# Kernel optimization log

Measured on AMD Instinct MI355X. Metric: run time of the kernel, lower is better.

The kernel has to match this reference:

```python
import jax, jax.numpy as jnp
import numpy as np

S, B, C, H = 1024, 4, 1024, 16
CC = C // H


def setup_inputs() -> dict:
    key = jax.random.key(0)
    ks = jax.random.split(key, 10)
    scale = 1.0 / np.sqrt(C)
    return {
        "x": jax.random.normal(ks[0], (S, B, C), dtype=jnp.float32),
        "r": jax.random.normal(ks[1], (S, B, C), dtype=jnp.float32),
        "Wq": jax.random.normal(ks[2], (C, C), dtype=jnp.float32) * scale,
        "bq": jnp.zeros((C,), dtype=jnp.float32),
        "Wke": jax.random.normal(ks[3], (C, C), dtype=jnp.float32) * scale,
        "bke": jnp.zeros((C,), dtype=jnp.float32),
        "Wkr": jax.random.normal(ks[4], (C, C), dtype=jnp.float32) * scale,
        "bkr": jnp.zeros((C,), dtype=jnp.float32),
        "u": jax.random.normal(ks[5], (C,), dtype=jnp.float32) * 0.02,
        "v": jax.random.normal(ks[6], (C,), dtype=jnp.float32) * 0.02,
    }


def reference(x, r, Wq, bq, Wke, bke, Wkr, bkr, u, v):
    s, b, c = x.shape
    h, cc = H, CC
    # projections (torch Linear: y = x @ W^T + b)
    ewq = (x @ Wq.T + bq).reshape(s, b, h, cc)
    ewke_full = x @ Wke.T + bke                 # [s,b,c]
    ewke = ewke_full.reshape(s, b, h, cc)
    rwkr_full = r @ Wkr.T + bkr                 # [s,b,c]
    rwkr = rwkr_full.reshape(s, b, h, cc)
    # content-content and content-position terms
    term_a = jnp.einsum('sbnc,tbnc->stbn', ewq, ewke)
    term_b = jnp.einsum('sbnc,tbnc->stbn', ewq, rwkr)
    # global bias terms: uwke/vwke are constant over (s,b), so the stb einsum
    # reduces to a tb contraction broadcast over s (same math, no s*b copies)
    uwke = Wke @ u + bke                        # [c]
    vwke = Wkr @ v + bkr                        # [c]
    term_c = jnp.einsum('c,tbc->tb', uwke, ewke_full)   # [t,b]
    term_d = jnp.einsum('c,tbc->tb', vwke, rwkr_full)   # [t,b]
    bias = (term_c + term_d)[None, :, :, None]          # [1,t,b,1]
    return term_a + term_b + bias               # [s,t,b,h]
```

## Files before the change

### kernel.cpp

```cpp
#include <hip/hip_runtime.h>
#include <hip/hip_bf16.h>
#include <stdint.h>

#define Ssz 1024
#define Bsz 4
#define Csz 1024
#define Hsz 16
#define Msz 4096

typedef unsigned short u16;
typedef __attribute__((ext_vector_type(8))) short bf16x8;
typedef __attribute__((ext_vector_type(8))) unsigned short u16x8;
typedef __attribute__((ext_vector_type(4))) float f32x4;
typedef __attribute__((ext_vector_type(4))) unsigned short u16x4;

__device__ __forceinline__ u16 f2bf(float f) {
  union { float f; unsigned u; } x; x.f = f;
  unsigned r = x.u + 0x7fffu + ((x.u >> 16) & 1u);
  return (u16)(r >> 16);
}

__device__ __forceinline__ void glds16(const void* g, void* l) {
  __builtin_amdgcn_global_load_lds(
      (__attribute__((address_space(1))) void*)g,
      (__attribute__((address_space(3))) void*)l, 16, 0, 0);
}

__device__ __forceinline__ int swzb(int x) { return x ^ (((x >> 8) & 7) << 4); }

__global__ __launch_bounds__(256) void k_convert_w(
    const float* __restrict__ Wq, const float* __restrict__ Wke, const float* __restrict__ Wkr,
    const float* __restrict__ bke, const float* __restrict__ bkr,
    const float* __restrict__ uu, const float* __restrict__ vv,
    u16* __restrict__ Bq, u16* __restrict__ B2, float* __restrict__ biasK,
    float* __restrict__ uwke, float* __restrict__ vwke) {
  int c = blockIdx.x;
  int tid = threadIdx.x;
  int c4 = tid * 4;
  float4 q = *(const float4*)(Wq + (size_t)c * Csz + c4);
  float4 e = *(const float4*)(Wke + (size_t)c * Csz + c4);
  float4 k = *(const float4*)(Wkr + (size_t)c * Csz + c4);
  u16x4 qo = { f2bf(q.x), f2bf(q.y), f2bf(q.z), f2bf(q.w) };
  u16x4 eo = { f2bf(e.x), f2bf(e.y), f2bf(e.z), f2bf(e.w) };
  u16x4 ko = { f2bf(k.x), f2bf(k.y), f2bf(k.z), f2bf(k.w) };
  *(u16x4*)(Bq + (size_t)c * 1024 + c4) = qo;
  *(u16x4*)(B2 + (size_t)c * 2048 + c4) = eo;
  *(u16x4*)(B2 + (size_t)c * 2048 + 1024 + c4) = ko;
  float4 u4 = *(const float4*)(uu + c4);
  float4 v4 = *(const float4*)(vv + c4);
  float se = e.x * u4.x + e.y * u4.y + e.z * u4.z + e.w * u4.w;
  float sk = k.x * v4.x + k.y * v4.y + k.z * v4.z + k.w * v4.w;
  for (int m = 32; m; m >>= 1) { se += __shfl_xor(se, m); sk += __shfl_xor(sk, m); }
  __shared__ float red[2][4];
  if ((tid & 63) == 0) { red[0][tid >> 6] = se; red[1][tid >> 6] = sk; }
  __syncthreads();
  if (tid == 0) {
    uwke[c] = red[0][0] + red[0][1] + red[0][2] + red[0][3] + bke[c];
    vwke[c] = red[1][0] + red[1][1] + red[1][2] + red[1][3] + bkr[c];
    biasK[c] = bke[c] + bkr[c];
  }
}

__global__ __launch_bounds__(256) void k_prep2(
    const float* __restrict__ Wke, const float* __restrict__ Wkr,
    const float* __restrict__ uwke, const float* __restrict__ vwke,
    const float* __restrict__ bke, const float* __restrict__ bkr,
    float* __restrict__ wu, float* __restrict__ wv, float* __restrict__ cst) {
  int bid = blockIdx.x;
  int tid = threadIdx.x;
  if (bid < 64) {
    const float* W = (bid < 32) ? Wke : Wkr;
    const float* sv = (bid < 32) ? uwke : vwke;
    float* o = (bid < 32) ? wu : wv;
    int d = (bid & 31) * 32 + (tid & 31);
    int cpar = tid >> 5;
    float acc = 0.f;
    #pragma unroll 8
    for (int c = cpar; c < Csz; c += 8) acc += sv[c] * W[(size_t)c * Csz + d];
    __shared__ float red[8][32];
    red[cpar][tid & 31] = acc;
    __syncthreads();
    if (cpar == 0) {
      float s = 0.f;
      #pragma unroll
      for (int i = 0; i < 8; i++) s += red[i][tid & 31];
      o[d] = s;
    }
  } else {
    float s = 0.f;
    for (int i = tid; i < Csz; i += 256) s += uwke[i] * bke[i] + vwke[i] * bkr[i];
    for (int m = 32; m; m >>= 1) s += __shfl_xor(s, m);
    __shared__ float red1[4];
    if ((tid & 63) == 0) red1[tid >> 6] = s;
    __syncthreads();
    if (tid == 0) cst[0] = red1[0] + red1[1] + red1[2] + red1[3];
  }
}

__global__ __launch_bounds__(256) void k_convert_xr_bias(
    const float* __restrict__ x, const float* __restrict__ r,
    const float* __restrict__ wu, const float* __restrict__ wv,
    const float* __restrict__ cst, u16* __restrict__ A2, float* __restrict__ biasTB) {
  int m = blockIdx.x;
  int tid = threadIdx.x;
  int c4 = tid * 4;
  float4 xv = *(const float4*)(x + (size_t)m * Csz + c4);
  float4 rv = *(const float4*)(r + (size_t)m * Csz + c4);
  u16x4 xo = { f2bf(xv.x), f2bf(xv.y), f2bf(xv.z), f2bf(xv.w) };
  u16x4 ro = { f2bf(rv.x), f2bf(rv.y), f2bf(rv.z), f2bf(rv.w) };
  *(u16x4*)(A2 + (size_t)m * 2048 + c4) = xo;
  *(u16x4*)(A2 + (size_t)m * 2048 + 1024 + c4) = ro;
  float4 a = *(const float4*)(wu + c4);
  float4 b = *(const float4*)(wv + c4);
  float s = xv.x * a.x + xv.y * a.y + xv.z * a.z + xv.w * a.w
          + rv.x * b.x + rv.y * b.y + rv.z * b.z + rv.w * b.w;
  for (int mm = 32; mm; mm >>= 1) s += __shfl_xor(s, mm);
  __shared__ float red[4];
  if ((tid & 63) == 0) red[tid >> 6] = s;
  __syncthreads();
  if (tid == 0) biasTB[m] = red[0] + red[1] + red[2] + red[3] + cst[0];
}

__global__ __launch_bounds__(256, 3) void k_gemm(
    const u16* __restrict__ A2, const u16* __restrict__ Bq, const u16* __restrict__ B2,
    const float* __restrict__ bq, const float* __restrict__ biasK,
    u16* __restrict__ QF, u16* __restrict__ KF) {
  __shared__ u16 smem[24576];

  const int z = blockIdx.z;
  const u16* A = A2; const int lda = 2048;
  const u16* B = (z == 0) ? Bq : B2;
  const int ldb = (z == 0) ? 1024 : 2048;
  const float* bias = (z == 0) ? bq : biasK;
  u16* OF = (z == 0) ? QF : KF;
  const int NT = ((z == 0) ? 1024 : 2048) >> 5;

  const int tid = threadIdx.x;
  const int bm = blockIdx.y * 128, bn = blockIdx.x * 128;
  const int wave = tid >> 6, lane = tid & 63;
  const int wm = (wave & 1) * 64, wn = (wave >> 1) * 64;
  const int fr = lane & 15, kg = (lane >> 4) * 8;

  const int ch0 = tid, ch1 = 256 + tid;
  const int r0 = ch0 >> 2, c0 = (ch0 & 3) * 8;
  const int r1 = ch1 >> 2, c1 = (ch1 & 3) * 8;
  const u16* a0 = A + (size_t)(bm + r0) * lda + c0;
  const u16* a1 = A + (size_t)(bm + r1) * lda + c1;
  const u16* b0 = B + (size_t)(bn + r0) * ldb + c0;
  const u16* b1 = B + (size_t)(bn + r1) * ldb + c1;

  f32x4 acc[4][4] = {};

  glds16(a0, smem + ch0 * 8);           glds16(a1, smem + ch1 * 8);
  glds16(b0, smem + 4096 + ch0 * 8);    glds16(b1, smem + 4096 + ch1 * 8);
  glds16(a0 + 32, smem + 8192 + ch0 * 8);        glds16(a1 + 32, smem + 8192 + ch1 * 8);
  glds16(b0 + 32, smem + 8192 + 4096 + ch0 * 8); glds16(b1 + 32, smem + 8192 + 4096 + ch1 * 8);

  int cur = 0;
  for (int t = 0; t < NT; t++) {
    if (t == NT - 1) {
      asm volatile("s_waitcnt vmcnt(0)" ::: "memory");
    } else {
      asm volatile("s_waitcnt vmcnt(4)" ::: "memory");
    }
    __builtin_amdgcn_s_barrier();
    asm volatile("" ::: "memory");
    if (t + 2 < NT) {
      const int nxt = cur >= 1 ? cur - 1 : 2;
      u16* an = smem + nxt * 8192;
      u16* bn_ = an + 4096;
      const int kt = (t + 2) * 32;
      glds16(a0 + kt, an + ch0 * 8);   glds16(a1 + kt, an + ch1 * 8);
      glds16(b0 + kt, bn_ + ch0 * 8);  glds16(b1 + kt, bn_ + ch1 * 8);
    }
    const u16* ac = smem + cur * 8192;
    const u16* bc = ac + 4096;
    bf16x8 af[4], bf[4];
    #pragma unroll
    for (int mi = 0; mi < 4; mi++) af[mi] = *(const bf16x8*)(ac + (wm + mi * 16 + fr) * 32 + kg);
    #pragma unroll
    for (int ni = 0; ni < 4; ni++) bf[ni] = *(const bf16x8*)(bc + (wn + ni * 16 + fr) * 32 + kg);
    #pragma unroll
    for (int mi = 0; mi < 4; mi++)
      #pragma unroll
      for (int ni = 0; ni < 4; ni++)
        acc[mi][ni] = __builtin_amdgcn_mfma_f32_16x16x32_bf16(af[mi], bf[ni], acc[mi][ni], 0, 0, 0);
    cur = cur < 2 ? cur + 1 : 0;
  }
  __syncthreads();

  const int hi = lane >> 4;
  const int e8 = fr & 7;
  const int fr3 = fr >> 3;
  u16* epw = smem + wave * 4096;
  float bvn[4];
  #pragma unroll
  for (int ni = 0; ni < 4; ni++) bvn[ni] = bias[bn + wn + ni * 16 + fr];
  #pragma unroll
  for (int ni = 0; ni < 4; ni++) {
    const int kk = ni >> 1;
    const int g = (ni * 2 + fr3) & 3;
    #pragma unroll
    for (int mi = 0; mi < 4; mi++) {
      const int inner = (g * 16 + mi * 4 + hi) * 8 + e8;
      #pragma unroll
      for (int j = 0; j < 4; j++)
        epw[(j * 2 + kk) * 512 + inner] = f2bf(acc[mi][ni][j] + bvn[ni]);
    }
  }
  const int s_tile = (bm >> 6) + (wm >> 6);
  const int nh = (bn + wn) >> 6;
  #pragma unroll
  for (int p = 0; p < 8; p++) {
    const int b2 = p >> 1, kk = p & 1;
    u16x8 v = *(const u16x8*)(&epw[p * 512 + lane * 8]);
    size_t ci = ((size_t)(s_tile * 4 + b2) * 16 + nh) * 2 + kk;
    *(u16x8*)(OF + ci * 512 + lane * 8) = v;
  }
}

__global__ __launch_bounds__(256, 3) void k_attn(
    const u16* __restrict__ QF, const u16* __restrict__ KF,
    const float* __restrict__ biasTB, float* __restrict__ out) {
  int id = blockIdx.x;
  int xcd = id & 7, within = id >> 3;
  int sx = xcd & 3, tx = xcd >> 2;
  int panel = within >> 7;
  int pl = within & 127;
  int s_tile = sx * 16 + (pl >> 3);
  int t_tile = tx * 32 + panel * 8 + (pl & 7);
  int s0 = s_tile * 16, t0 = t_tile * 16;

  int tid = threadIdx.x;
  int wave = tid >> 6, lane = tid & 63;
  int fr = lane & 15;

  const u16* qp = QF + (size_t)(s_tile * 4 + wave) * 16384 + lane * 8;
  const u16* kp = KF + (size_t)(t_tile * 4 + wave) * 16384 + lane * 8;

  f32x4 acc[16];
  #pragma unroll
  for (int n = 0; n < 16; n++) acc[n] = (f32x4){0.f, 0.f, 0.f, 0.f};

  #pragma unroll
  for (int n = 0; n < 16; n++) {
    #pragma unroll
    for (int kk = 0; kk < 2; kk++) {
      bf16x8 a  = *(const bf16x8*)(qp + (n * 2 + kk) * 512);
      bf16x8 bb = *(const bf16x8*)(kp + (n * 2 + kk) * 512);
      acc[n] = __builtin_amdgcn_mfma_f32_16x16x32_bf16(a, bb, acc[n], 0, 0, 0);
    }
  }

  __shared__ float lds[8192];
  float bv = biasTB[(t0 + (tid >> 4)) * 4 + ((tid >> 2) & 3)];
  int hi = (lane >> 4) & 1;
  int myg = (lane >> 4) >> 1;

  #pragma unroll
  for (int g = 0; g < 2; g++) {
    __syncthreads();
    if (myg == g) {
      #pragma unroll
      for (int j = 0; j < 4; j++) {
        int lbase = (((hi * 4 + j) * 16 + fr) * 4 + wave) * 64;
        #pragma unroll
        for (int n0 = 0; n0 < 16; n0 += 4) {
          f32x4 v = { acc[n0][j], acc[n0 + 1][j], acc[n0 + 2][j], acc[n0 + 3][j] };
          *(f32x4*)((char*)lds + swzb(lbase + n0 * 4)) = v;
        }
      }
    }
    __syncthreads();
    #pragma unroll
    for (int sr = 0; sr < 8; sr++) {
      f32x4 v = *(const f32x4*)((char*)lds + swzb(sr * 4096 + tid * 16));
      v += bv;
      size_t off = ((size_t)(s0 + g * 8 + sr) * 1024 + t0) * 64 + tid * 4;
      __builtin_nontemporal_store(v, (f32x4*)(out + off));
    }
  }
}

extern "C" void kernel_launch(void* const* d_in, const int* in_sizes, int n_in,
                              void* d_out, int out_size, void* d_ws, size_t ws_size,
                              hipStream_t stream) {
  const float* x   = (const float*)d_in[0];
  const float* r   = (const float*)d_in[1];
  const float* Wq  = (const float*)d_in[2];
  const float* bq  = (const float*)d_in[3];
  const float* Wke = (const float*)d_in[4];
  const float* bke = (const float*)d_in[5];
  const float* Wkr = (const float*)d_in[6];
  const float* bkr = (const float*)d_in[7];
  const float* uu  = (const float*)d_in[8];
  const float* vv  = (const float*)d_in[9];
  float* out = (float*)d_out;
  char* ws = (char*)d_ws;

  u16* A2 = (u16*)(ws + 0);
  u16* QF = (u16*)(ws + 16777216);
  u16* KF = (u16*)(ws + 25165824);
  u16* B2 = (u16*)(ws + 33554432);
  u16* Bq = (u16*)(ws + 37748736);
  float* uwke  = (float*)(ws + 39845888);
  float* vwke  = (float*)(ws + 39849984);
  float* wu    = (float*)(ws + 39854080);
  float* wv    = (float*)(ws + 39858176);
  float* biasK = (float*)(ws + 39862272);
  float* cst   = (float*)(ws + 39866368);
  float* biasTB = (float*)(ws + 39866624);

  k_convert_w<<<1024, 256, 0, stream>>>(Wq, Wke, Wkr, bke, bkr, uu, vv,
                                        Bq, B2, biasK, uwke, vwke);
  k_prep2<<<65, 256, 0, stream>>>(Wke, Wkr, uwke, vwke, bke, bkr, wu, wv, cst);
  k_convert_xr_bias<<<4096, 256, 0, stream>>>(x, r, wu, wv, cst, A2, biasTB);
  k_gemm<<<dim3(8, 32, 2), 256, 0, stream>>>(A2, Bq, B2, bq, biasK, QF, KF);
  k_attn<<<4096, 256, 0, stream>>>(QF, KF, biasTB, out);
}
```

Before: 126.9 us.

## Compute two t-tiles per attention block to reuse Q fragments

Each k_attn block now computes a 16x32 (s,t) tile instead of 16x16, loading each Q fragment once and applying it to two K tiles, and the grid is halved to 2048 blocks. The epilogue is restructured into four LDS staging passes, each covering four s rows by 32 t columns, with separate bias values for the two t halves. This cuts redundant Q loads and per-block overhead, at the cost of double the accumulator registers (which can lower occupancy under launch_bounds 256,3) and more LDS sync rounds. The kernel is dominated by output stores, so the benefit is limited.

```diff
diff --git a/kernel.cpp b/kernel.cpp
--- a/kernel.cpp
+++ b/kernel.cpp
@@ -225,58 +225,70 @@
   int id = blockIdx.x;
   int xcd = id & 7, within = id >> 3;
   int sx = xcd & 3, tx = xcd >> 2;
-  int panel = within >> 7;
-  int pl = within & 127;
-  int s_tile = sx * 16 + (pl >> 3);
-  int t_tile = tx * 32 + panel * 8 + (pl & 7);
-  int s0 = s_tile * 16, t0 = t_tile * 16;
+  int panel = within >> 6;
+  int pl = within & 63;
+  int s_tile = sx * 16 + (pl >> 2);
+  int t2 = tx * 16 + panel * 4 + (pl & 3);
+  int s0 = s_tile * 16;
 
   int tid = threadIdx.x;
   int wave = tid >> 6, lane = tid & 63;
   int fr = lane & 15;
 
-  const u16* qp = QF + (size_t)(s_tile * 4 + wave) * 16384 + lane * 8;
-  const u16* kp = KF + (size_t)(t_tile * 4 + wave) * 16384 + lane * 8;
-
-  f32x4 acc[16];
-  #pragma unroll
-  for (int n = 0; n < 16; n++) acc[n] = (f32x4){0.f, 0.f, 0.f, 0.f};
-
+  const u16* qp  = QF + (size_t)(s_tile * 4 + wave) * 16384 + lane * 8;
+  const u16* kpA = KF + (size_t)((t2 * 2) * 4 + wave) * 16384 + lane * 8;
+  const u16* kpB = kpA + 4 * 16384;
+
+  f32x4 accA[16], accB[16];
   #pragma unroll
   for (int n = 0; n < 16; n++) {
-    #pragma unroll
-    for (int kk = 0; kk < 2; kk++) {
-      bf16x8 a  = *(const bf16x8*)(qp + (n * 2 + kk) * 512);
-      bf16x8 bb = *(const bf16x8*)(kp + (n * 2 + kk) * 512);
-      acc[n] = __builtin_amdgcn_mfma_f32_16x16x32_bf16(a, bb, acc[n], 0, 0, 0);
-    }
+    accA[n] = (f32x4){0.f, 0.f, 0.f, 0.f};
+    accB[n] = (f32x4){0.f, 0.f, 0.f, 0.f};
+  }
+
+  #pragma unroll
+  for (int n = 0; n < 16; n++) {
+    bf16x8 q0 = *(const bf16x8*)(qp + (n * 2 + 0) * 512);
+    bf16x8 q1 = *(const bf16x8*)(qp + (n * 2 + 1) * 512);
+    bf16x8 a0 = *(const bf16x8*)(kpA + (n * 2 + 0) * 512);
+    bf16x8 a1 = *(const bf16x8*)(kpA + (n * 2 + 1) * 512);
+    bf16x8 b0 = *(const bf16x8*)(kpB + (n * 2 + 0) * 512);
+    bf16x8 b1 = *(const bf16x8*)(kpB + (n * 2 + 1) * 512);
+    accA[n] = __builtin_amdgcn_mfma_f32_16x16x32_bf16(q0, a0, accA[n], 0, 0, 0);
+    accA[n] = __builtin_amdgcn_mfma_f32_16x16x32_bf16(q1, a1, accA[n], 0, 0, 0);
+    accB[n] = __builtin_amdgcn_mfma_f32_16x16x32_bf16(q0, b0, accB[n], 0, 0, 0);
+    accB[n] = __builtin_amdgcn_mfma_f32_16x16x32_bf16(q1, b1, accB[n], 0, 0, 0);
   }
 
   __shared__ float lds[8192];
-  float bv = biasTB[(t0 + (tid >> 4)) * 4 + ((tid >> 2) & 3)];
-  int hi = (lane >> 4) & 1;
-  int myg = (lane >> 4) >> 1;
-
-  #pragma unroll
-  for (int g = 0; g < 2; g++) {
+  float bv0 = biasTB[(t2 * 32 +      (tid >> 4)) * 4 + ((tid >> 2) & 3)];
+  float bv1 = biasTB[(t2 * 32 + 16 + (tid >> 4)) * 4 + ((tid >> 2) & 3)];
+  int hi = lane >> 4;
+
+  #pragma unroll
+  for (int p = 0; p < 4; p++) {
     __syncthreads();
-    if (myg == g) {
+    if (hi == p) {
       #pragma unroll
       for (int j = 0; j < 4; j++) {
-        int lbase = (((hi * 4 + j) * 16 + fr) * 4 + wave) * 64;
+        int lbaseA = ((j * 32 +      fr) * 4 + wave) * 64;
+        int lbaseB = ((j * 32 + 16 + fr) * 4 + wave) * 64;
         #pragma unroll
         for (int n0 = 0; n0 < 16; n0 += 4) {
-          f32x4 v = { acc[n0][j], acc[n0 + 1][j], acc[n0 + 2][j], acc[n0 + 3][j] };
-          *(f32x4*)((char*)lds + swzb(lbase + n0 * 4)) = v;
+          f32x4 vA = { accA[n0][j], accA[n0 + 1][j], accA[n0 + 2][j], accA[n0 + 3][j] };
+          f32x4 vB = { accB[n0][j], accB[n0 + 1][j], accB[n0 + 2][j], accB[n0 + 3][j] };
+          *(f32x4*)((char*)lds + swzb(lbaseA + n0 * 4)) = vA;
+          *(f32x4*)((char*)lds + swzb(lbaseB + n0 * 4)) = vB;
         }
       }
     }
     __syncthreads();
     #pragma unroll
-    for (int sr = 0; sr < 8; sr++) {
-      f32x4 v = *(const f32x4*)((char*)lds + swzb(sr * 4096 + tid * 16));
-      v += bv;
-      size_t off = ((size_t)(s0 + g * 8 + sr) * 1024 + t0) * 64 + tid * 4;
+    for (int i = 0; i < 8; i++) {
+      f32x4 v = *(const f32x4*)((char*)lds + swzb(i * 4096 + tid * 16));
+      v += (i & 1) ? bv1 : bv0;
+      size_t off = ((size_t)(s0 + p * 4 + (i >> 1)) * 1024 + t2 * 32) * 64
+                   + (i & 1) * 1024 + tid * 4;
       __builtin_nontemporal_store(v, (f32x4*)(out + off));
     }
   }
@@ -316,5 +328,5 @@
   k_prep2<<<65, 256, 0, stream>>>(Wke, Wkr, uwke, vwke, bke, bkr, wu, wv, cst);
   k_convert_xr_bias<<<4096, 256, 0, stream>>>(x, r, wu, wv, cst, A2, biasTB);
   k_gemm<<<dim3(8, 32, 2), 256, 0, stream>>>(A2, Bq, B2, bq, biasK, QF, KF);
-  k_attn<<<4096, 256, 0, stream>>>(QF, KF, biasTB, out);
-}
+  k_attn<<<2048, 256, 0, stream>>>(QF, KF, biasTB, out);
+}
```

After: 135.7 us. 1.07x slower.
